# Kernel optimization log

Measured on AMD Instinct MI355X. Metric: run time of the kernel, lower is better.

The kernel has to match this reference:

```python
import jax, jax.numpy as jnp
import numpy as np

D_ENC = 512
D_DEC = 512
JOINT = 512
VOCAB = 1024


def setup_inputs() -> dict:
    key = jax.random.key(0)
    ks = jax.random.split(key, 7)
    B, T, U = 4, 256, 64
    s_enc = 1.0 / np.sqrt(D_ENC)
    s_dec = 1.0 / np.sqrt(D_DEC)
    s_out = 1.0 / np.sqrt(JOINT)
    return {
        "encoder_out": jax.random.normal(ks[0], (B, T, 1, D_ENC), dtype=jnp.float32),
        "decoder_out": jax.random.normal(ks[1], (B, 1, U, D_DEC), dtype=jnp.float32),
        # torch.nn.Linear stores weight as (out, in); uniform(-1/sqrt(in), 1/sqrt(in))
        "W_enc": jax.random.uniform(ks[2], (JOINT, D_ENC), jnp.float32, -s_enc, s_enc),
        "b_enc": jax.random.uniform(ks[3], (JOINT,), jnp.float32, -s_enc, s_enc),
        "W_dec": jax.random.uniform(ks[4], (JOINT, D_DEC), jnp.float32, -s_dec, s_dec),
        "W_out": jax.random.uniform(ks[5], (VOCAB, JOINT), jnp.float32, -s_out, s_out),
        "b_out": jax.random.uniform(ks[6], (VOCAB,), jnp.float32, -s_out, s_out),
    }


def reference(encoder_out, decoder_out, W_enc, b_enc, W_dec, W_out, b_out):
    # Project each side in its small shape first (B,T,1,J) and (B,1,U,J),
    # then broadcast-add over (T,U), tanh, output GEMM -> (B,T,U,V).
    enc = jnp.einsum("btud,jd->btuj", encoder_out, W_enc) + b_enc  # (B,T,1,J)
    dec = jnp.einsum("btud,jd->btuj", decoder_out, W_dec)          # (B,1,U,J)
    h = jnp.tanh(enc + dec)                                        # (B,T,U,J)
    return jnp.einsum("btuj,vj->btuv", h, W_out) + b_out           # (B,T,U,V)
```

## Files before the change

kernel.cpp:

```cpp
#include <hip/hip_runtime.h>
#include <hip/hip_bf16.h>


typedef __attribute__((ext_vector_type(8))) short short8;
typedef __attribute__((ext_vector_type(4))) float f32x4;
typedef __attribute__((ext_vector_type(8))) float f32x8;
typedef __attribute__((ext_vector_type(16))) float f32x16;

#define SZ0 524288
#define SZ1 131072
#define SZ2 262144
#define SZ3 512
#define SZ4 262144
#define SZ5 524288
#define SZ6 1024
#define CU0 0
#define CU1 524288
#define CU2 655360
#define CU3 917504
#define CU4 918016
#define CU5 1180160
#define CU6 1704448
#define CTOT 1705472

__global__ void detect_kernel(const void* p0, const void* p1, const void* p2,
                              const void* p3, const void* p4, const void* p5,
                              const void* p6, int* flags) {
  const void* ps[7] = {p0, p1, p2, p3, p4, p5, p6};
  const int sz[7] = {SZ0, SZ1, SZ2, SZ3, SZ4, SZ5, SZ6};
  const int w = threadIdx.x >> 6;
  const int l = threadIdx.x & 63;
  if (w >= 7) return;
  const unsigned short* u = (const unsigned short*)ps[w];
  const int lim = sz[w] < 1024 ? sz[w] : 1024;
  int bad = 0;
  for (int j = l; j < lim; j += 64) {
    const unsigned e = (u[j] >> 7) & 0xFFu;
    if (e >= 0x8Eu) bad = 1;
  }
  const unsigned long long b = __ballot(bad);
  if (l == 0) flags[w] = (b != 0ULL) ? 1 : 0;
}

__global__ __launch_bounds__(256) void convert_kernel(
    const void* p0, const void* p1, const void* p2, const void* p3,
    const void* p4, const void* p5, const void* p6,
    const int* __restrict__ flags, __hip_bfloat16* __restrict__ dst) {
  const int gid = blockIdx.x * 256 + threadIdx.x;
  if (gid >= CTOT) return;
  int t, local;
  const void* p;
  if (gid < CU1)      { t = 0; local = gid - CU0; p = p0; }
  else if (gid < CU2) { t = 1; local = gid - CU1; p = p1; }
  else if (gid < CU3) { t = 2; local = gid - CU2; p = p2; }
  else if (gid < CU4) { t = 3; local = gid - CU3; p = p3; }
  else if (gid < CU5) { t = 4; local = gid - CU4; p = p4; }
  else if (gid < CU6) { t = 5; local = gid - CU5; p = p5; }
  else                { t = 6; local = gid - CU6; p = p6; }
  __hip_bfloat16 v;
  if (flags[t])
    v = __float2bfloat16(((const float*)p)[local]);
  else
    v = ((const __hip_bfloat16*)p)[local];
  dst[gid] = v;
}

__device__ __forceinline__ void gemm_bt_body(
    const __hip_bfloat16* __restrict__ A, const __hip_bfloat16* __restrict__ Bw,
    const __hip_bfloat16* __restrict__ bias, float* __restrict__ C,
    int M, int N, int K, int bid,
    __hip_bfloat16* sA, __hip_bfloat16* sB) {
  const int tid = threadIdx.x;
  const int w = tid >> 6;
  const int l = tid & 63;
  const int ntiles = N >> 7;
  const int mt = bid / ntiles;
  const int nt = bid % ntiles;
  const int m0 = mt << 7;
  const int n0 = nt << 7;
  const int wm = (w >> 1) << 6;
  const int wn = (w & 1) << 6;
  const int r16 = l & 15;
  const int q = l >> 4;

  f32x4 acc[4][4] = {};

  const int srow_in = l >> 3;
  const int scol = (l & 7) << 3;

  for (int k0 = 0; k0 < K; k0 += 64) {
#pragma unroll
    for (int i = 0; i < 4; ++i) {
      const int c = (w << 2) + i;
      const int row = (c << 3) + srow_in;
      const __hip_bfloat16* gA = A + (size_t)(m0 + row) * K + k0 + scol;
      const __hip_bfloat16* gB = Bw + (size_t)(n0 + row) * K + k0 + scol;
      __builtin_amdgcn_global_load_lds(
          (const __attribute__((address_space(1))) void*)gA,
          (__attribute__((address_space(3))) void*)(sA + (c << 9) + (l << 3)),
          16, 0, 0);
      __builtin_amdgcn_global_load_lds(
          (const __attribute__((address_space(1))) void*)gB,
          (__attribute__((address_space(3))) void*)(sB + (c << 9) + (l << 3)),
          16, 0, 0);
    }
    __syncthreads();

#pragma unroll
    for (int kk = 0; kk < 2; ++kk) {
      const int kc = (kk << 5) + (q << 3);
      short8 af[4], bf[4];
#pragma unroll
      for (int mi = 0; mi < 4; ++mi)
        af[mi] = *(const short8*)(sA + (wm + (mi << 4) + r16) * 64 + kc);
#pragma unroll
      for (int ni = 0; ni < 4; ++ni)
        bf[ni] = *(const short8*)(sB + (wn + (ni << 4) + r16) * 64 + kc);
#pragma unroll
      for (int mi = 0; mi < 4; ++mi)
#pragma unroll
        for (int ni = 0; ni < 4; ++ni)
          acc[mi][ni] = __builtin_amdgcn_mfma_f32_16x16x32_bf16(
              af[mi], bf[ni], acc[mi][ni], 0, 0, 0);
    }
    __syncthreads();
  }

#pragma unroll
  for (int ni = 0; ni < 4; ++ni) {
    const int col = n0 + wn + (ni << 4) + r16;
    const float bc = bias ? __bfloat162float(bias[col]) : 0.0f;
#pragma unroll
    for (int mi = 0; mi < 4; ++mi) {
      const int rowb = m0 + wm + (mi << 4) + (q << 2);
#pragma unroll
      for (int i = 0; i < 4; ++i)
        C[(size_t)(rowb + i) * N + col] = acc[mi][ni][i] + bc;
    }
  }
}

__global__ __launch_bounds__(256) void proj_kernel(
    const __hip_bfloat16* __restrict__ enc, const __hip_bfloat16* __restrict__ Wenc,
    const __hip_bfloat16* __restrict__ benc,
    const __hip_bfloat16* __restrict__ dec, const __hip_bfloat16* __restrict__ Wdec,
    const __hip_bfloat16* __restrict__ Wout, __hip_bfloat16* __restrict__ WT,
    float* __restrict__ Pe, float* __restrict__ Pd) {
  __shared__ __align__(16) __hip_bfloat16 sA[128 * 64];
  __shared__ __align__(16) __hip_bfloat16 sB[128 * 64];
  if (blockIdx.x < 32) {
    gemm_bt_body(enc, Wenc, benc, Pe, 1024, 512, 512, blockIdx.x, sA, sB);
  } else if (blockIdx.x < 40) {
    gemm_bt_body(dec, Wdec, nullptr, Pd, 256, 512, 512, blockIdx.x - 32, sA, sB);
  } else {
    const int bid = blockIdx.x - 40;
#pragma unroll
    for (int i = 0; i < 32; ++i) {
      const int cid = (bid << 13) + (i << 8) + threadIdx.x;
      const int n = cid >> 6;
      const int c = cid & 63;
      *(short8*)(WT + (((size_t)c << 10) + n) * 8) =
          *(const short8*)(Wout + (size_t)n * 512 + (c << 3));
    }
  }
}

__global__ __launch_bounds__(512, 4) void gemm_joint(
    const float* __restrict__ Pe, const float* __restrict__ Pd,
    const __hip_bfloat16* __restrict__ WT,
    const __hip_bfloat16* __restrict__ bias, float* __restrict__ out) {
  __shared__ __align__(16) __hip_bfloat16 sH[16 * 128 * 8];
  __shared__ __align__(16) __hip_bfloat16 sB[2][4 * 256 * 8];

  const int t = threadIdx.x;
  const int w = t >> 6;
  const int l = t & 63;
  const int l31 = l & 31;
  const int q2 = l >> 5;
  const int mb = blockIdx.x >> 2;
  const int nb = blockIdx.x & 3;
  const int m0 = mb << 7;
  const int n0 = nb << 8;

  auto stage = [&](int kt, int b) {
#pragma unroll
    for (int h = 0; h < 2; ++h) {
      const int slot = (h << 9) + t;
      const int kq = slot >> 8;
      const int n = slot & 255;
      const __hip_bfloat16* src =
          WT + (((size_t)((kt << 2) + kq) << 10) + n0 + n) * 8;
      __builtin_amdgcn_global_load_lds(
          (const __attribute__((address_space(1))) void*)src,
          (__attribute__((address_space(3))) void*)(&sB[b][0] + (slot << 3)),
          16, 0, 0);
    }
  };

  auto fillH = [&](int q) {
    const int r = t & 127;
    const int e = (mb << 1) + (r >> 6);
    const int d = ((mb >> 7) << 6) | (r & 63);
    const float* peR = Pe + (size_t)e * 512 + (q << 7);
    const float* pdR = Pd + (size_t)d * 512 + (q << 7);
#pragma unroll
    for (int s2 = 0; s2 < 4; ++s2) {
      const int cq = (s2 << 2) + (t >> 7);
      const f32x8 a = *(const f32x8*)(peR + (cq << 3));
      const f32x8 bv = *(const f32x8*)(pdR + (cq << 3));
      short8 hv;
#pragma unroll
      for (int x = 0; x < 8; ++x) {
        const float sv = a[x] + bv[x];
        const float u = __expf(2.0f * sv);
        const float tv = 1.0f - 2.0f * __builtin_amdgcn_rcpf(u + 1.0f);
        const __hip_bfloat16 hb = __float2bfloat16(tv);
        hv[x] = *(const short*)&hb;
      }
      *(short8*)(sH + ((size_t)((cq << 7) + r) << 3)) = hv;
    }
  };

  stage(0, 0);
  fillH(0);
  __syncthreads();

  const int wm = (w >> 2) << 6;
  const int wn = (w & 3) << 6;
  f32x16 acc[2][2] = {};

  for (int kt = 0; kt < 16; ++kt) {
    const int b = kt & 1;
    if (kt < 15) {
      stage(kt + 1, b ^ 1);
      asm volatile("s_waitcnt vmcnt(2)" ::: "memory");
    } else {
      asm volatile("s_waitcnt vmcnt(0)" ::: "memory");
    }
    __builtin_amdgcn_sched_barrier(0);
    __builtin_amdgcn_s_barrier();
    __builtin_amdgcn_sched_barrier(0);

    if ((kt & 3) == 0 && kt) {
      fillH(kt >> 2);
      asm volatile("s_waitcnt lgkmcnt(0)" ::: "memory");
      __builtin_amdgcn_sched_barrier(0);
      __builtin_amdgcn_s_barrier();
      __builtin_amdgcn_sched_barrier(0);
    }

#pragma unroll
    for (int ss = 0; ss < 2; ++ss) {
      const int kq = (ss << 1) + q2;
      const int cq = ((kt & 3) << 2) + kq;
      short8 af[2], bf[2];
#pragma unroll
      for (int mi = 0; mi < 2; ++mi)
        af[mi] = *(const short8*)(sH +
                                  (((cq << 7) + wm + (mi << 5) + l31) << 3));
#pragma unroll
      for (int ni = 0; ni < 2; ++ni)
        bf[ni] = *(const short8*)(&sB[b][0] +
                                  (((kq << 8) + wn + (ni << 5) + l31) << 3));
#pragma unroll
      for (int mi = 0; mi < 2; ++mi)
#pragma unroll
        for (int ni = 0; ni < 2; ++ni)
          acc[mi][ni] = __builtin_amdgcn_mfma_f32_32x32x16_bf16(
              af[mi], bf[ni], acc[mi][ni], 0, 0, 0);
    }

    __builtin_amdgcn_sched_barrier(0);
    __builtin_amdgcn_s_barrier();
    __builtin_amdgcn_sched_barrier(0);
  }

#pragma unroll
  for (int ni = 0; ni < 2; ++ni) {
    const int col = n0 + wn + (ni << 5) + l31;
    const float bc = __bfloat162float(bias[col]);
#pragma unroll
    for (int mi = 0; mi < 2; ++mi) {
#pragma unroll
      for (int rr = 0; rr < 16; ++rr) {
        const int row = m0 + wm + (mi << 5) + (rr & 3) + ((rr >> 2) << 3) +
                        (q2 << 2);
        out[(size_t)row * 1024 + col] = acc[mi][ni][rr] + bc;
      }
    }
  }
}

extern "C" void kernel_launch(void* const* d_in, const int* in_sizes, int n_in,
                              void* d_out, int out_size, void* d_ws,
                              size_t ws_size, hipStream_t stream) {
  char* ws = (char*)d_ws;
  int* flags = (int*)ws;
  __hip_bfloat16* cp = (__hip_bfloat16*)(ws + 256);
  float* Pe = (float*)(ws + (4ull << 20));
  float* Pd = (float*)(ws + (6ull << 20));
  __hip_bfloat16* WT = (__hip_bfloat16*)(ws + (8ull << 20));

  detect_kernel<<<dim3(1), dim3(512), 0, stream>>>(
      d_in[0], d_in[1], d_in[2], d_in[3], d_in[4], d_in[5], d_in[6], flags);
  convert_kernel<<<dim3((CTOT + 255) / 256), dim3(256), 0, stream>>>(
      d_in[0], d_in[1], d_in[2], d_in[3], d_in[4], d_in[5], d_in[6], flags, cp);

  const __hip_bfloat16* enc_c = cp + CU0;
  const __hip_bfloat16* dec_c = cp + CU1;
  const __hip_bfloat16* Wenc_c = cp + CU2;
  const __hip_bfloat16* benc_c = cp + CU3;
  const __hip_bfloat16* Wdec_c = cp + CU4;
  const __hip_bfloat16* Wout_c = cp + CU5;
  const __hip_bfloat16* bout_c = cp + CU6;

  proj_kernel<<<dim3(48), dim3(256), 0, stream>>>(
      enc_c, Wenc_c, benc_c, dec_c, Wdec_c, Wout_c, WT, Pe, Pd);
  gemm_joint<<<dim3(2048), dim3(512), 0, stream>>>(
      Pe, Pd, WT, bout_c, (float*)d_out);
}
```

Before: 392.9 us.

## Retile joint GEMM to 64x512 with full-K H tile and triple-buffered weights

Switches the joint GEMM block tile from 128x256 to 64x512. The whole 64xK tanh activation tile is computed once up front instead of in four chunks with extra barriers, and each M block now maps to a single (b,t) row. Weight staging moves to a three-stage ring with two tiles in flight, and the MFMA section is wrapped in s_setprio. In exchange, LDS use per block grows (64 KB for H plus 96 KB for weights), so only one block fits per CU. Each output tile also reuses W_out across fewer rows, which raises weight traffic.

```diff
diff --git a/kernel.cpp b/kernel.cpp
--- a/kernel.cpp
+++ b/kernel.cpp
@@ -165,49 +165,46 @@
   }
 }
 
-__global__ __launch_bounds__(512, 4) void gemm_joint(
+__global__ __launch_bounds__(512, 2) void gemm_joint(
     const float* __restrict__ Pe, const float* __restrict__ Pd,
     const __hip_bfloat16* __restrict__ WT,
     const __hip_bfloat16* __restrict__ bias, float* __restrict__ out) {
-  __shared__ __align__(16) __hip_bfloat16 sH[16 * 128 * 8];
-  __shared__ __align__(16) __hip_bfloat16 sB[2][4 * 256 * 8];
+  __shared__ __align__(16) __hip_bfloat16 sH[64 * 64 * 8];
+  __shared__ __align__(16) __hip_bfloat16 sB[3][4 * 512 * 8];
 
   const int t = threadIdx.x;
   const int w = t >> 6;
   const int l = t & 63;
   const int l31 = l & 31;
   const int q2 = l >> 5;
-  const int mb = blockIdx.x >> 2;
-  const int nb = blockIdx.x & 3;
-  const int m0 = mb << 7;
-  const int n0 = nb << 8;
+  const int mb = blockIdx.x >> 1;
+  const int nb = blockIdx.x & 1;
+  const int m0 = mb << 6;
+  const int n0 = nb << 9;
 
   auto stage = [&](int kt, int b) {
 #pragma unroll
-    for (int h = 0; h < 2; ++h) {
-      const int slot = (h << 9) + t;
-      const int kq = slot >> 8;
-      const int n = slot & 255;
+    for (int h = 0; h < 4; ++h) {
       const __hip_bfloat16* src =
-          WT + (((size_t)((kt << 2) + kq) << 10) + n0 + n) * 8;
+          WT + (((size_t)((kt << 2) + h) << 10) + n0 + t) * 8;
       __builtin_amdgcn_global_load_lds(
           (const __attribute__((address_space(1))) void*)src,
-          (__attribute__((address_space(3))) void*)(&sB[b][0] + (slot << 3)),
+          (__attribute__((address_space(3))) void*)(
+              &sB[b][0] + (((h << 9) + t) << 3)),
           16, 0, 0);
     }
   };
 
-  auto fillH = [&](int q) {
-    const int r = t & 127;
-    const int e = (mb << 1) + (r >> 6);
-    const int d = ((mb >> 7) << 6) | (r & 63);
-    const float* peR = Pe + (size_t)e * 512 + (q << 7);
-    const float* pdR = Pd + (size_t)d * 512 + (q << 7);
-#pragma unroll
-    for (int s2 = 0; s2 < 4; ++s2) {
-      const int cq = (s2 << 2) + (t >> 7);
-      const f32x8 a = *(const f32x8*)(peR + (cq << 3));
-      const f32x8 bv = *(const f32x8*)(pdR + (cq << 3));
+  stage(0, 0);
+  stage(1, 1);
+  {
+    const float* peR = Pe + (size_t)mb * 512;
+    const float* pdR = Pd + (size_t)(((mb >> 8) << 6) | l) * 512;
+#pragma unroll
+    for (int j = 0; j < 8; ++j) {
+      const int c = (j << 3) + w;
+      const f32x8 a = *(const f32x8*)(peR + (c << 3));
+      const f32x8 bv = *(const f32x8*)(pdR + (c << 3));
       short8 hv;
 #pragma unroll
       for (int x = 0; x < 8; ++x) {
@@ -217,23 +214,25 @@
         const __hip_bfloat16 hb = __float2bfloat16(tv);
         hv[x] = *(const short*)&hb;
       }
-      *(short8*)(sH + ((size_t)((cq << 7) + r) << 3)) = hv;
-    }
-  };
-
-  stage(0, 0);
-  fillH(0);
-  __syncthreads();
-
-  const int wm = (w >> 2) << 6;
-  const int wn = (w & 3) << 6;
+      *(short8*)(sH + ((size_t)((c << 6) + l) << 3)) = hv;
+    }
+  }
+  asm volatile("s_waitcnt lgkmcnt(0)" ::: "memory");
+  __builtin_amdgcn_sched_barrier(0);
+  __builtin_amdgcn_s_barrier();
+  __builtin_amdgcn_sched_barrier(0);
+
+  const int wn = w << 6;
   f32x16 acc[2][2] = {};
+  int bs = 2;
+  int br = 0;
 
   for (int kt = 0; kt < 16; ++kt) {
-    const int b = kt & 1;
-    if (kt < 15) {
-      stage(kt + 1, b ^ 1);
-      asm volatile("s_waitcnt vmcnt(2)" ::: "memory");
+    if (kt <= 13) {
+      stage(kt + 2, bs);
+      asm volatile("s_waitcnt vmcnt(8)" ::: "memory");
+    } else if (kt == 14) {
+      asm volatile("s_waitcnt vmcnt(4)" ::: "memory");
     } else {
       asm volatile("s_waitcnt vmcnt(0)" ::: "memory");
     }
@@ -241,27 +240,19 @@
     __builtin_amdgcn_s_barrier();
     __builtin_amdgcn_sched_barrier(0);
 
-    if ((kt & 3) == 0 && kt) {
-      fillH(kt >> 2);
-      asm volatile("s_waitcnt lgkmcnt(0)" ::: "memory");
-      __builtin_amdgcn_sched_barrier(0);
-      __builtin_amdgcn_s_barrier();
-      __builtin_amdgcn_sched_barrier(0);
-    }
-
+    __builtin_amdgcn_s_setprio(1);
 #pragma unroll
     for (int ss = 0; ss < 2; ++ss) {
-      const int kq = (ss << 1) + q2;
-      const int cq = ((kt & 3) << 2) + kq;
+      const int c = (kt << 2) + (ss << 1) + q2;
+      const int kc = (ss << 1) + q2;
       short8 af[2], bf[2];
 #pragma unroll
       for (int mi = 0; mi < 2; ++mi)
-        af[mi] = *(const short8*)(sH +
-                                  (((cq << 7) + wm + (mi << 5) + l31) << 3));
+        af[mi] = *(const short8*)(sH + (((c << 6) + (mi << 5) + l31) << 3));
 #pragma unroll
       for (int ni = 0; ni < 2; ++ni)
-        bf[ni] = *(const short8*)(&sB[b][0] +
-                                  (((kq << 8) + wn + (ni << 5) + l31) << 3));
+        bf[ni] = *(const short8*)(&sB[br][0] +
+                                  (((kc << 9) + wn + (ni << 5) + l31) << 3));
 #pragma unroll
       for (int mi = 0; mi < 2; ++mi)
 #pragma unroll
@@ -269,10 +260,14 @@
           acc[mi][ni] = __builtin_amdgcn_mfma_f32_32x32x16_bf16(
               af[mi], bf[ni], acc[mi][ni], 0, 0, 0);
     }
+    __builtin_amdgcn_s_setprio(0);
 
     __builtin_amdgcn_sched_barrier(0);
     __builtin_amdgcn_s_barrier();
     __builtin_amdgcn_sched_barrier(0);
+
+    br = (br == 2) ? 0 : br + 1;
+    bs = (bs == 2) ? 0 : bs + 1;
   }
 
 #pragma unroll
@@ -283,8 +278,7 @@
     for (int mi = 0; mi < 2; ++mi) {
 #pragma unroll
       for (int rr = 0; rr < 16; ++rr) {
-        const int row = m0 + wm + (mi << 5) + (rr & 3) + ((rr >> 2) << 3) +
-                        (q2 << 2);
+        const int row = m0 + (mi << 5) + (rr & 3) + ((rr >> 2) << 3) + (q2 << 2);
         out[(size_t)row * 1024 + col] = acc[mi][ni][rr] + bc;
       }
     }
```

After: 420.7 us. 7.1% more time.

## Enlarge joint GEMM tile to 256x256 with register-prefetched tanh A pipeline

Applied to the files above, without the earlier changes.

The joint GEMM block tile grows from 128x256 to 256x256, halving the grid and doubling per-wave accumulators (4x2 MFMA tiles). The tanh activation tile is now double-buffered: the next K-slice's Pe/Pd values are prefetched into registers while the current slice is multiplied, then converted and written to LDS. W loads are spread across the phases, and s_setprio raises priority around the MFMA bursts. The goal is more operand reuse per LDS read and hiding the activation and load latency behind matrix work, at the cost of higher register pressure, lower occupancy and more barriers.

```diff
diff --git a/kernel.cpp b/kernel.cpp
--- a/kernel.cpp
+++ b/kernel.cpp
@@ -4,7 +4,6 @@
 
 typedef __attribute__((ext_vector_type(8))) short short8;
 typedef __attribute__((ext_vector_type(4))) float f32x4;
-typedef __attribute__((ext_vector_type(8))) float f32x8;
 typedef __attribute__((ext_vector_type(16))) float f32x16;
 
 #define SZ0 524288
@@ -165,12 +164,12 @@
   }
 }
 
-__global__ __launch_bounds__(512, 4) void gemm_joint(
+__global__ __launch_bounds__(512, 2) void gemm_joint(
     const float* __restrict__ Pe, const float* __restrict__ Pd,
     const __hip_bfloat16* __restrict__ WT,
     const __hip_bfloat16* __restrict__ bias, float* __restrict__ out) {
-  __shared__ __align__(16) __hip_bfloat16 sH[16 * 128 * 8];
-  __shared__ __align__(16) __hip_bfloat16 sB[2][4 * 256 * 8];
+  __shared__ __align__(16) __hip_bfloat16 sA[2][2048 * 8];
+  __shared__ __align__(16) __hip_bfloat16 sB[2][2048 * 8];
 
   const int t = threadIdx.x;
   const int w = t >> 6;
@@ -179,108 +178,153 @@
   const int q2 = l >> 5;
   const int mb = blockIdx.x >> 2;
   const int nb = blockIdx.x & 3;
-  const int m0 = mb << 7;
+  const int m0 = mb << 8;
   const int n0 = nb << 8;
-
-  auto stage = [&](int kt, int b) {
-#pragma unroll
-    for (int h = 0; h < 2; ++h) {
-      const int slot = (h << 9) + t;
-      const int kq = slot >> 8;
-      const int n = slot & 255;
-      const __hip_bfloat16* src =
-          WT + (((size_t)((kt << 2) + kq) << 10) + n0 + n) * 8;
-      __builtin_amdgcn_global_load_lds(
-          (const __attribute__((address_space(1))) void*)src,
-          (__attribute__((address_space(3))) void*)(&sB[b][0] + (slot << 3)),
-          16, 0, 0);
+  const int wm = (w >> 2) << 7;
+  const int wn = (w & 3) << 6;
+
+  const int arow = t & 255;
+  const int acb = (t >> 8) << 2;
+  const int e = (mb << 2) + (arow >> 6);
+  const int dd = ((mb >> 6) << 6) | (arow & 63);
+
+  f32x4 rPe[4][2], rPd[4][2];
+  auto issueA = [&](int kt) {
+    const float* peR = Pe + (size_t)e * 512 + (kt << 6);
+    const float* pdR = Pd + (size_t)dd * 512 + (kt << 6);
+#pragma unroll
+    for (int j = 0; j < 4; ++j) {
+      const int off = (acb + j) << 3;
+      rPe[j][0] = *(const f32x4*)(peR + off);
+      rPe[j][1] = *(const f32x4*)(peR + off + 4);
+      rPd[j][0] = *(const f32x4*)(pdR + off);
+      rPd[j][1] = *(const f32x4*)(pdR + off + 4);
     }
   };
 
-  auto fillH = [&](int q) {
-    const int r = t & 127;
-    const int e = (mb << 1) + (r >> 6);
-    const int d = ((mb >> 7) << 6) | (r & 63);
-    const float* peR = Pe + (size_t)e * 512 + (q << 7);
-    const float* pdR = Pd + (size_t)d * 512 + (q << 7);
-#pragma unroll
-    for (int s2 = 0; s2 < 4; ++s2) {
-      const int cq = (s2 << 2) + (t >> 7);
-      const f32x8 a = *(const f32x8*)(peR + (cq << 3));
-      const f32x8 bv = *(const f32x8*)(pdR + (cq << 3));
+  auto writeA = [&](int b) {
+#pragma unroll
+    for (int j = 0; j < 4; ++j) {
       short8 hv;
 #pragma unroll
-      for (int x = 0; x < 8; ++x) {
-        const float sv = a[x] + bv[x];
-        const float u = __expf(2.0f * sv);
-        const float tv = 1.0f - 2.0f * __builtin_amdgcn_rcpf(u + 1.0f);
-        const __hip_bfloat16 hb = __float2bfloat16(tv);
+      for (int x = 0; x < 4; ++x) {
+        float sv = rPe[j][0][x] + rPd[j][0][x];
+        float u = __expf(2.0f * sv);
+        float tv = 1.0f - 2.0f * __builtin_amdgcn_rcpf(u + 1.0f);
+        __hip_bfloat16 hb = __float2bfloat16(tv);
         hv[x] = *(const short*)&hb;
+        sv = rPe[j][1][x] + rPd[j][1][x];
+        u = __expf(2.0f * sv);
+        tv = 1.0f - 2.0f * __builtin_amdgcn_rcpf(u + 1.0f);
+        hb = __float2bfloat16(tv);
+        hv[4 + x] = *(const short*)&hb;
       }
-      *(short8*)(sH + ((size_t)((cq << 7) + r) << 3)) = hv;
+      *(short8*)(&sA[b][0] + ((((acb + j) << 8) + arow) << 3)) = hv;
     }
   };
 
-  stage(0, 0);
-  fillH(0);
-  __syncthreads();
-
-  const int wm = (w >> 2) << 6;
-  const int wn = (w & 3) << 6;
-  f32x16 acc[2][2] = {};
-
-  for (int kt = 0; kt < 16; ++kt) {
+  auto issueB = [&](int kt, int b, int h) {
+    const int slot = (h << 9) + t;
+    const int c = slot >> 8;
+    const int n = slot & 255;
+    const __hip_bfloat16* src =
+        WT + (((size_t)((kt << 3) + c) << 10) + n0 + n) * 8;
+    __builtin_amdgcn_global_load_lds(
+        (const __attribute__((address_space(1))) void*)src,
+        (__attribute__((address_space(3))) void*)(&sB[b][0] + (slot << 3)),
+        16, 0, 0);
+  };
+
+  issueA(0);
+#pragma unroll
+  for (int h = 0; h < 4; ++h) issueB(0, 0, h);
+  asm volatile("s_waitcnt vmcnt(4)" ::: "memory");
+  __builtin_amdgcn_sched_barrier(0);
+  writeA(0);
+  asm volatile("s_waitcnt lgkmcnt(0) vmcnt(0)" ::: "memory");
+  __builtin_amdgcn_sched_barrier(0);
+  __builtin_amdgcn_s_barrier();
+  __builtin_amdgcn_sched_barrier(0);
+
+  f32x16 acc[4][2] = {};
+
+#define READS(s)                                                             \
+  {                                                                          \
+    const int c = ((s) << 1) + q2;                                           \
+    _Pragma("unroll") for (int mi = 0; mi < 4; ++mi) af[mi] =                \
+        *(const short8*)(&sA[b][0] +                                         \
+                         (((c << 8) + wm + (mi << 5) + l31) << 3));          \
+    _Pragma("unroll") for (int ni = 0; ni < 2; ++ni) bf[ni] =                \
+        *(const short8*)(&sB[b][0] +                                         \
+                         (((c << 8) + wn + (ni << 5) + l31) << 3));          \
+  }
+#define MFMA8                                                                \
+  _Pragma("unroll") for (int mi = 0; mi < 4; ++mi)                           \
+      _Pragma("unroll") for (int ni = 0; ni < 2; ++ni) acc[mi][ni] =         \
+          __builtin_amdgcn_mfma_f32_32x32x16_bf16(af[mi], bf[ni],            \
+                                                  acc[mi][ni], 0, 0, 0);
+#define PHASE_SYNC_PRE                                                       \
+  __builtin_amdgcn_s_barrier();                                              \
+  asm volatile("s_waitcnt lgkmcnt(0)" ::: "memory");                         \
+  __builtin_amdgcn_sched_barrier(0);                                         \
+  __builtin_amdgcn_s_setprio(1);
+#define PHASE_SYNC_POST                                                      \
+  __builtin_amdgcn_s_setprio(0);                                             \
+  __builtin_amdgcn_sched_barrier(0);                                         \
+  __builtin_amdgcn_s_barrier();                                              \
+  __builtin_amdgcn_sched_barrier(0);
+
+#pragma unroll
+  for (int kt = 0; kt < 8; ++kt) {
     const int b = kt & 1;
-    if (kt < 15) {
-      stage(kt + 1, b ^ 1);
-      asm volatile("s_waitcnt vmcnt(2)" ::: "memory");
-    } else {
-      asm volatile("s_waitcnt vmcnt(0)" ::: "memory");
-    }
+    short8 af[4], bf[2];
+
+    if (kt < 7) issueA(kt + 1);
+    READS(0)
+    PHASE_SYNC_PRE
+    MFMA8
+    PHASE_SYNC_POST
+
+    if (kt < 7) { issueB(kt + 1, b ^ 1, 0); issueB(kt + 1, b ^ 1, 1); }
+    READS(1)
+    PHASE_SYNC_PRE
+    MFMA8
+    PHASE_SYNC_POST
+
+    if (kt < 7) { issueB(kt + 1, b ^ 1, 2); issueB(kt + 1, b ^ 1, 3); }
+    READS(2)
+    PHASE_SYNC_PRE
+    MFMA8
+    PHASE_SYNC_POST
+
+    READS(3)
+    if (kt < 7) {
+      asm volatile("s_waitcnt vmcnt(4)" ::: "memory");
+      __builtin_amdgcn_sched_barrier(0);
+      writeA(b ^ 1);
+    }
+    __builtin_amdgcn_s_barrier();
+    asm volatile("s_waitcnt lgkmcnt(0)" ::: "memory");
+    __builtin_amdgcn_sched_barrier(0);
+    __builtin_amdgcn_s_setprio(1);
+    MFMA8
+    __builtin_amdgcn_s_setprio(0);
+    asm volatile("s_waitcnt vmcnt(0)" ::: "memory");
     __builtin_amdgcn_sched_barrier(0);
     __builtin_amdgcn_s_barrier();
     __builtin_amdgcn_sched_barrier(0);
-
-    if ((kt & 3) == 0 && kt) {
-      fillH(kt >> 2);
-      asm volatile("s_waitcnt lgkmcnt(0)" ::: "memory");
-      __builtin_amdgcn_sched_barrier(0);
-      __builtin_amdgcn_s_barrier();
-      __builtin_amdgcn_sched_barrier(0);
-    }
-
-#pragma unroll
-    for (int ss = 0; ss < 2; ++ss) {
-      const int kq = (ss << 1) + q2;
-      const int cq = ((kt & 3) << 2) + kq;
-      short8 af[2], bf[2];
-#pragma unroll
-      for (int mi = 0; mi < 2; ++mi)
-        af[mi] = *(const short8*)(sH +
-                                  (((cq << 7) + wm + (mi << 5) + l31) << 3));
-#pragma unroll
-      for (int ni = 0; ni < 2; ++ni)
-        bf[ni] = *(const short8*)(&sB[b][0] +
-                                  (((kq << 8) + wn + (ni << 5) + l31) << 3));
-#pragma unroll
-      for (int mi = 0; mi < 2; ++mi)
-#pragma unroll
-        for (int ni = 0; ni < 2; ++ni)
-          acc[mi][ni] = __builtin_amdgcn_mfma_f32_32x32x16_bf16(
-              af[mi], bf[ni], acc[mi][ni], 0, 0, 0);
-    }
-
-    __builtin_amdgcn_sched_barrier(0);
-    __builtin_amdgcn_s_barrier();
-    __builtin_amdgcn_sched_barrier(0);
-  }
+  }
+#undef READS
+#undef MFMA8
+#undef PHASE_SYNC_PRE
+#undef PHASE_SYNC_POST
 
 #pragma unroll
   for (int ni = 0; ni < 2; ++ni) {
     const int col = n0 + wn + (ni << 5) + l31;
     const float bc = __bfloat162float(bias[col]);
 #pragma unroll
-    for (int mi = 0; mi < 2; ++mi) {
+    for (int mi = 0; mi < 4; ++mi) {
 #pragma unroll
       for (int rr = 0; rr < 16; ++rr) {
         const int row = m0 + wm + (mi << 5) + (rr & 3) + ((rr >> 2) << 3) +
@@ -316,6 +360,6 @@
 
   proj_kernel<<<dim3(48), dim3(256), 0, stream>>>(
       enc_c, Wenc_c, benc_c, dec_c, Wdec_c, Wout_c, WT, Pe, Pd);
-  gemm_joint<<<dim3(2048), dim3(512), 0, stream>>>(
+  gemm_joint<<<dim3(1024), dim3(512), 0, stream>>>(
       Pe, Pd, WT, bout_c, (float*)d_out);
 }
```

Result: slower. 436.0 us (+11.0%).
